# Optimization experiments

Hardware: AMD Instinct MI355X
Metric: run time of the kernel (lower is better)

Reference implementation:

```python
import jax, jax.numpy as jnp
import numpy as np

DIM = 192
HEADS = 6
HIDDEN = 384  # int(DIM * 2.0)


def _ln(x, w, b):
    # WithBias LayerNorm over channel dim (torch normalizes last dim of b,(hw),c)
    mu = jnp.mean(x, axis=1, keepdims=True)
    var = jnp.var(x, axis=1, keepdims=True)
    return (x - mu) / jnp.sqrt(var + 1e-5) * w[None, :, None, None] + b[None, :, None, None]


def _conv1x1(x, w):  # w: [O, I, 1, 1]
    return jnp.einsum('bihw,oi->bohw', x, w[:, :, 0, 0])


def _dwconv3(x, w):  # depthwise 3x3, w: [C, 1, 3, 3]
    return jax.lax.conv_general_dilated(
        x, w, window_strides=(1, 1), padding=((1, 1), (1, 1)),
        feature_group_count=x.shape[1],
        dimension_numbers=('NCHW', 'OIHW', 'NCHW'))


def _l2norm(x):  # F.normalize along last axis
    n = jnp.sqrt(jnp.sum(x * x, axis=-1, keepdims=True))
    return x / jnp.maximum(n, 1e-12)


def setup_inputs() -> dict:
    key = jax.random.key(0)
    ks = jax.random.split(key, 16)
    s = 0.02
    d = {}
    d['x'] = jax.random.normal(ks[0], (2, DIM, 128, 128), dtype=jnp.float32)
    d['k_v'] = jax.random.normal(ks[1], (2, 256), dtype=jnp.float32)
    d['ln1_w'] = jnp.ones((DIM,), jnp.float32)
    d['ln1_b'] = jnp.zeros((DIM,), jnp.float32)
    d['temp'] = jnp.ones((HEADS, 1, 1), jnp.float32)
    d['w_kR'] = jax.random.normal(ks[2], (DIM * 3 // 4, 192), jnp.float32) * s
    d['w_kI'] = jax.random.normal(ks[3], (DIM // 4, 64), jnp.float32) * s
    d['w_qR'] = jax.random.normal(ks[4], (DIM, DIM * 3 // 4, 1, 1), jnp.float32) * s
    d['w_qdw'] = jax.random.normal(ks[5], (DIM, 1, 3, 3), jnp.float32) * s
    d['w_kvI'] = jax.random.normal(ks[6], (DIM * 2, DIM // 4, 1, 1), jnp.float32) * s
    d['w_kvdw'] = jax.random.normal(ks[7], (DIM * 2, 1, 3, 3), jnp.float32) * s
    d['w_po'] = jax.random.normal(ks[8], (DIM, DIM, 1, 1), jnp.float32) * s
    d['ln2_w'] = jnp.ones((DIM,), jnp.float32)
    d['ln2_b'] = jnp.zeros((DIM,), jnp.float32)
    d['w_ffk'] = jax.random.normal(ks[9], (DIM, 256), jnp.float32) * s
    d['w_pin'] = jax.random.normal(ks[10], (HIDDEN * 2, DIM, 1, 1), jnp.float32) * s
    d['w_dw'] = jax.random.normal(ks[11], (HIDDEN * 2, 1, 3, 3), jnp.float32) * s
    d['w_pout'] = jax.random.normal(ks[12], (DIM, HIDDEN, 1, 1), jnp.float32) * s
    return d


def reference(x, k_v, ln1_w, ln1_b, temp, w_kR, w_kI, w_qR, w_qdw, w_kvI, w_kvdw,
              w_po, ln2_w, ln2_b, w_ffk, w_pin, w_dw, w_pout):
    b, c, h, w = x.shape
    c3 = c * 3 // 4
    # ---- Rttention on norm1(x) ----
    xn = _ln(x, ln1_w, ln1_b)
    kvr = (k_v[:, :192] @ w_kR.T)[:, :, None, None]   # [b, 3c/4, 1, 1]
    kvi = (k_v[:, 192:] @ w_kI.T)[:, :, None, None]   # [b, c/4, 1, 1]
    x_r = xn[:, :c3] * kvr + xn[:, :c3]
    x_i = xn[:, c3:] * kvi + xn[:, c3:]
    q = _dwconv3(_conv1x1(x_r, w_qR), w_qdw)          # [b, c, h, w]
    kv = _dwconv3(_conv1x1(x_i, w_kvI), w_kvdw)       # [b, 2c, h, w]
    k, v = jnp.split(kv, 2, axis=1)
    rh = lambda t: t.reshape(b, HEADS, c // HEADS, h * w)
    q = _l2norm(rh(q))
    k = _l2norm(rh(k))
    v = rh(v)
    # channel-wise attention: [b, head, c_h, c_h]
    attn = jax.nn.softmax(jnp.einsum('bhcd,bhed->bhce', q, k) * temp[None], axis=-1)
    out = jnp.einsum('bhce,bhed->bhcd', attn, v).reshape(b, c, h, w)
    x = x + _conv1x1(out, w_po)
    # ---- GDFN FeedForward on norm2(x) ----
    xn2 = _ln(x, ln2_w, ln2_b)
    kvf = (k_v @ w_ffk.T)[:, :, None, None]           # [b, c, 1, 1]
    y = xn2 * kvf + xn2
    y = _dwconv3(_conv1x1(y, w_pin), w_dw)            # [b, 2*hidden, h, w]
    y1, y2 = jnp.split(y, 2, axis=1)
    y = jax.nn.gelu(y1, approximate=False) * y2
    x = x + _conv1x1(y, w_pout)
    return (x, k_v)
```

## Files before the change

kernel.cpp:

```cpp
#include <hip/hip_runtime.h>
#include <math.h>

#define HW 16384
#define CDIM 192
#define C3 144
#define C4 48
#define NB 2
#define NPX 32768
#define HEADS 6

typedef unsigned short u16;
typedef unsigned int u32;
typedef __attribute__((ext_vector_type(8))) short bf16x8;
typedef __attribute__((ext_vector_type(4))) float f32x4;

__device__ __forceinline__ float bf2f(u16 u) {
    return __uint_as_float(((unsigned int)u) << 16);
}
__device__ __forceinline__ u16 f2bf(float f) {
    unsigned int x = __float_as_uint(f);
    unsigned int r = x + 0x7fffu + ((x >> 16) & 1u);
    return (u16)(r >> 16);
}

static inline float* wsf(void* ws, size_t off) { return (float*)((char*)ws + off); }
static inline u16* wsh(void* ws, size_t off) { return (u16*)((char*)ws + off); }

__global__ void k_setup(const float* __restrict__ kvv, const float* __restrict__ wkR,
                        const float* __restrict__ wkI, const float* __restrict__ wffk,
                        const float* __restrict__ wqR, const float* __restrict__ wkvI,
                        const float* __restrict__ wpo, const float* __restrict__ wpin,
                        const float* __restrict__ wpout,
                        const float* __restrict__ ln2w, const float* __restrict__ ln2b,
                        u16* __restrict__ wb, float* __restrict__ sm,
                        float* __restrict__ A2, float* __restrict__ B2,
                        float* __restrict__ tail) {
    int t = blockIdx.x * 256 + threadIdx.x;
    if (t < 313344) {
        float v;
        if (t < 30720) {
            int o = t / 160, i = t % 160;
            v = (i < 144) ? wqR[o * 144 + i] : 0.f;
        } else if (t < 55296) {
            int r = t - 30720; int o = r / 64, i = r % 64;
            v = (i < 48) ? wkvI[o * 48 + i] : 0.f;
        } else if (t < 92160) {
            v = wpo[t - 55296];
        } else if (t < 239616) {
            v = wpin[t - 92160];
        } else {
            v = wpout[t - 239616];
        }
        wb[t] = f2bf(v);
    } else if (t < 314112) {
        int r = t - 313344;
        if (r < 288) {
            int b = r / 144, o = r % 144;
            const float* v = kvv + b * 256;
            const float* w = wkR + o * 192;
            float s = 0.f;
            for (int j = 0; j < 192; j++) s += v[j] * w[j];
            sm[r] = s + 1.0f;
        } else if (r < 384) {
            int r2 = r - 288;
            int b = r2 / 48, o = r2 % 48;
            const float* v = kvv + b * 256 + 192;
            const float* w = wkI + o * 64;
            float s = 0.f;
            for (int j = 0; j < 64; j++) s += v[j] * w[j];
            sm[288 + r2] = s + 1.0f;
        } else {
            int r2 = r - 384;
            int b = r2 / 192, o = r2 % 192;
            const float* v = kvv + b * 256;
            const float* w = wffk + o * 256;
            float s = 0.f;
            for (int j = 0; j < 256; j++) s += v[j] * w[j];
            float sc = s + 1.0f;
            sm[384 + r2] = sc;
            A2[r2] = ln2w[o] * sc;
            B2[r2] = ln2b[o] * sc;
        }
    } else if (t < 314624) {
        int r = t - 314112;
        tail[r] = kvv[r];
    }
}

__global__ __launch_bounds__(256) void k_ln1(
    const float* __restrict__ xin,
    const float* __restrict__ lnw, const float* __restrict__ lnb,
    const float* __restrict__ sca, const float* __restrict__ scb,
    u16* __restrict__ outA, u16* __restrict__ outB) {
    __shared__ float red[2][16][16][4];
    __shared__ float mu_s[16][4], rstd_s[16][4];
    int t = threadIdx.x;
    int px4 = t & 15, cg = t >> 4;
    int base = blockIdx.x * 64;
    int b = base >> 14;
    int p = (base & 16383) + px4 * 4;
    float vals[12][4];
    float s[4] = {0.f, 0.f, 0.f, 0.f}, s2[4] = {0.f, 0.f, 0.f, 0.f};
#pragma unroll
    for (int j = 0; j < 12; j++) {
        int c = cg * 12 + j;
        size_t off = ((size_t)(b * CDIM + c)) * HW + p;
        float4 f = *(const float4*)(xin + off);
        float v[4] = {f.x, f.y, f.z, f.w};
#pragma unroll
        for (int q = 0; q < 4; q++) {
            vals[j][q] = v[q]; s[q] += v[q]; s2[q] += v[q] * v[q];
        }
    }
#pragma unroll
    for (int q = 0; q < 4; q++) { red[0][cg][px4][q] = s[q]; red[1][cg][px4][q] = s2[q]; }
    __syncthreads();
    if (t < 16) {
        float S[4] = {0.f, 0.f, 0.f, 0.f}, S2[4] = {0.f, 0.f, 0.f, 0.f};
        for (int g2 = 0; g2 < 16; g2++)
#pragma unroll
            for (int q = 0; q < 4; q++) { S[q] += red[0][g2][t][q]; S2[q] += red[1][g2][t][q]; }
#pragma unroll
        for (int q = 0; q < 4; q++) {
            float mu = S[q] * (1.0f / CDIM);
            float var = S2[q] * (1.0f / CDIM) - mu * mu;
            mu_s[t][q] = mu;
            rstd_s[t][q] = rsqrtf(var + 1e-5f);
        }
    }
    __syncthreads();
    float mu[4], rs[4];
#pragma unroll
    for (int q = 0; q < 4; q++) { mu[q] = mu_s[px4][q]; rs[q] = rstd_s[px4][q]; }
    float Ac[12], Bc[12];
#pragma unroll
    for (int j = 0; j < 12; j++) {
        int c = cg * 12 + j;
        float sc = (c < C3) ? sca[b * C3 + c] : scb[b * C4 + (c - C3)];
        Ac[j] = lnw[c] * sc;
        Bc[j] = lnb[c] * sc;
    }
    int isR = (cg < 12);
    size_t row0 = (size_t)b * HW + p;
    u16* basep = isR ? (outA + row0 * 160 + cg * 12)
                     : (outB + row0 * 64 + (cg * 12 - 144));
    int rowlen = isR ? 160 : 64;
#pragma unroll
    for (int q = 0; q < 4; q++) {
        u16 tmp[12];
#pragma unroll
        for (int j = 0; j < 12; j++)
            tmp[j] = f2bf((vals[j][q] - mu[q]) * rs[q] * Ac[j] + Bc[j]);
        u16* op = basep + q * rowlen;
        ushort4 o0 = {tmp[0], tmp[1], tmp[2], tmp[3]};
        ushort4 o1 = {tmp[4], tmp[5], tmp[6], tmp[7]};
        ushort4 o2 = {tmp[8], tmp[9], tmp[10], tmp[11]};
        *(ushort4*)(op) = o0;
        *(ushort4*)(op + 4) = o1;
        *(ushort4*)(op + 8) = o2;
    }
    if (cg == 0) {
        int4 z = {0, 0, 0, 0};
#pragma unroll
        for (int q = 0; q < 4; q++) {
            u16* pr = outA + (row0 + q) * 160 + 144;
            *(int4*)(pr) = z; *(int4*)(pr + 8) = z;
            u16* pi = outB + (row0 + q) * 64 + 48;
            *(int4*)(pi) = z; *(int4*)(pi + 8) = z;
        }
    }
}

template <int NCH, int MODE>
__global__ __launch_bounds__(256) void k_gemm_t(
    const u16* __restrict__ X, const u16* __restrict__ Wb,
    const void* __restrict__ resid, void* __restrict__ outp, int CO) {
    constexpr int CIP = NCH * 32;
    __shared__ __align__(16) u16 Xs[128 * 40];
    __shared__ __align__(16) u16 Wsh[64 * 40];
    const int tid = threadIdx.x;
    const int n0 = blockIdx.x * 128;
    const int m0 = blockIdx.y * 64;
    const int b = blockIdx.z;
    const int wave = tid >> 6, lane = tid & 63;
    const int quad = lane >> 4, l16 = lane & 15;
    const int spx = tid >> 1, sh = tid & 1;
    const int swr = tid >> 2, swc = tid & 3;
    const u16* xsrc = X + ((size_t)b * HW + n0 + spx) * CIP + sh * 16;
    const u16* wsrc = Wb + (size_t)(m0 + swr) * CIP + swc * 8;
    int4 xr0 = *(const int4*)(xsrc);
    int4 xr1 = *(const int4*)(xsrc + 8);
    int4 wr0 = *(const int4*)(wsrc);
    f32x4 acc[4][2] = {};
#pragma unroll
    for (int ch = 0; ch < NCH; ch++) {
        if (ch) __syncthreads();
        *(int4*)&Xs[spx * 40 + sh * 16] = xr0;
        *(int4*)&Xs[spx * 40 + sh * 16 + 8] = xr1;
        *(int4*)&Wsh[swr * 40 + swc * 8] = wr0;
        if (ch + 1 < NCH) {
            xr0 = *(const int4*)(xsrc + (ch + 1) * 32);
            xr1 = *(const int4*)(xsrc + (ch + 1) * 32 + 8);
            wr0 = *(const int4*)(wsrc + (ch + 1) * 32);
        }
        __syncthreads();
        bf16x8 af[4];
#pragma unroll
        for (int mi = 0; mi < 4; mi++)
            af[mi] = *(const bf16x8*)&Wsh[(mi * 16 + l16) * 40 + quad * 8];
        bf16x8 bf0 = *(const bf16x8*)&Xs[(wave * 32 + l16) * 40 + quad * 8];
        bf16x8 bf1 = *(const bf16x8*)&Xs[(wave * 32 + 16 + l16) * 40 + quad * 8];
#pragma unroll
        for (int mi = 0; mi < 4; mi++) {
            acc[mi][0] = __builtin_amdgcn_mfma_f32_16x16x32_bf16(af[mi], bf0, acc[mi][0], 0, 0, 0);
            acc[mi][1] = __builtin_amdgcn_mfma_f32_16x16x32_bf16(af[mi], bf1, acc[mi][1], 0, 0, 0);
        }
    }
#pragma unroll
    for (int mi = 0; mi < 4; mi++) {
#pragma unroll
        for (int ni = 0; ni < 2; ni++) {
            int c0 = m0 + mi * 16 + quad * 4;
            int px = n0 + wave * 32 + ni * 16 + l16;
            if (MODE == 0) {
                u16* ob = (u16*)outp + ((size_t)b * CO + c0) * HW + px;
#pragma unroll
                for (int rr = 0; rr < 4; rr++) ob[(size_t)rr * HW] = f2bf(acc[mi][ni][rr]);
            } else {
                const float* rp = (const float*)resid + ((size_t)b * 192 + c0) * HW + px;
                ushort4 o;
                o.x = f2bf(acc[mi][ni][0] + rp[0]);
                o.y = f2bf(acc[mi][ni][1] + rp[(size_t)HW]);
                o.z = f2bf(acc[mi][ni][2] + rp[(size_t)2 * HW]);
                o.w = f2bf(acc[mi][ni][3] + rp[(size_t)3 * HW]);
                *(ushort4*)((u16*)outp + ((size_t)b * HW + px) * 192 + c0) = o;
            }
        }
    }
}

__global__ __launch_bounds__(256) void k_gemm_s(
    const u16* __restrict__ X, const u16* __restrict__ Wb,
    const u16* __restrict__ residT, float* __restrict__ outp) {
    constexpr int NCH = 12;
    constexpr int CIP = NCH * 32;
    __shared__ __align__(16) u16 Ws[64 * 32];
    __shared__ __align__(16) u16 Xs[32 * 130];
    const int tid = threadIdx.x;
    const int n0 = blockIdx.x * 128;
    const int m0 = blockIdx.y * 64;
    const int b = blockIdx.z;
    const u16* Xb = X + (size_t)b * 384 * HW + n0;
    const int wave = tid >> 6, lane = tid & 63;
    const int quad = lane >> 4, l16 = lane & 15;
    const int smr = tid >> 2, sk4 = tid & 3;
    const int skr = tid >> 3, sc0 = (tid & 7) * 16;
    f32x4 acc[4][2] = {};
    for (int ch = 0; ch < NCH; ch++) {
        const int k0 = ch * 32;
        if (ch) __syncthreads();
        {
            const int4 wv = *(const int4*)(Wb + (size_t)(m0 + smr) * CIP + k0 + sk4 * 8);
            *(int4*)&Ws[(smr << 5) + (((sk4 ^ (smr & 3)) & 3) << 3)] = wv;
        }
        {
            const u16* xc = Xb + (size_t)(k0 + skr) * HW + sc0;
            int4 r0 = *(const int4*)xc;
            int4 r1 = *(const int4*)(xc + 8);
            u32* dst = (u32*)&Xs[skr * 130 + sc0];
#pragma unroll
            for (int i = 0; i < 4; i++) dst[i] = ((const u32*)&r0)[i];
#pragma unroll
            for (int i = 0; i < 4; i++) dst[4 + i] = ((const u32*)&r1)[i];
        }
        __syncthreads();
        bf16x8 af[4];
#pragma unroll
        for (int mi = 0; mi < 4; mi++) {
            int row = mi * 16 + l16;
            af[mi] = *(const bf16x8*)&Ws[(row << 5) + ((quad ^ (row & 3)) << 3)];
        }
#pragma unroll
        for (int ni = 0; ni < 2; ni++) {
            int n = wave * 32 + ni * 16 + l16;
            bf16x8 bfr;
#pragma unroll
            for (int j = 0; j < 8; j++) bfr[j] = (short)Xs[(quad * 8 + j) * 130 + n];
#pragma unroll
            for (int mi = 0; mi < 4; mi++)
                acc[mi][ni] = __builtin_amdgcn_mfma_f32_16x16x32_bf16(af[mi], bfr, acc[mi][ni], 0, 0, 0);
        }
    }
#pragma unroll
    for (int mi = 0; mi < 4; mi++) {
#pragma unroll
        for (int ni = 0; ni < 2; ni++) {
            int c0 = m0 + mi * 16 + quad * 4;
            int px = n0 + wave * 32 + ni * 16 + l16;
            ushort4 rv = *(const ushort4*)(residT + ((size_t)b * HW + px) * 192 + c0);
            float* ob = outp + ((size_t)b * 192 + c0) * HW + px;
            ob[0] = acc[mi][ni][0] + bf2f(rv.x);
            ob[(size_t)HW] = acc[mi][ni][1] + bf2f(rv.y);
            ob[(size_t)2 * HW] = acc[mi][ni][2] + bf2f(rv.z);
            ob[(size_t)3 * HW] = acc[mi][ni][3] + bf2f(rv.w);
        }
    }
}

__global__ __launch_bounds__(256) void k_dw2(const u16* __restrict__ X,
                                             const float* __restrict__ Wd,
                                             u16* __restrict__ out, int C, int sqCh,
                                             float* __restrict__ sqp) {
    __shared__ float In[34 * 132];
    __shared__ float red[4];
    int bc = blockIdx.x >> 2, rt = blockIdx.x & 3;
    int b = bc / C, ch = bc % C;
    const u16* xb = X + (size_t)bc * HW;
    int t = threadIdx.x;
    int c0 = (t & 7) * 16;
    for (int r = t >> 3; r < 34; r += 32) {
        int y = rt * 32 - 1 + r;
        float* dst = &In[r * 132 + 1 + c0];
        if ((unsigned)y < 128u) {
            const u16* src = xb + y * 128 + c0;
            int4 r0 = *(const int4*)src;
            int4 r1 = *(const int4*)(src + 8);
            const u16* p0 = (const u16*)&r0;
            const u16* p1 = (const u16*)&r1;
#pragma unroll
            for (int i = 0; i < 8; i++) dst[i] = bf2f(p0[i]);
#pragma unroll
            for (int i = 0; i < 8; i++) dst[8 + i] = bf2f(p1[i]);
        } else {
#pragma unroll
            for (int i = 0; i < 16; i++) dst[i] = 0.f;
        }
    }
    if (t < 34) { In[t * 132] = 0.f; In[t * 132 + 129] = 0.f; }
    __syncthreads();
    const float* w = Wd + ch * 9;
    float w00 = w[0], w01 = w[1], w02 = w[2], w10 = w[3], w11 = w[4],
          w12 = w[5], w20 = w[6], w21 = w[7], w22 = w[8];
    int x = t & 127, rg = t >> 7;
    int base = rg * 16;
    float A2 = 0.f, A1 = 0.f, B1 = 0.f, ssq = 0.f;
    u16* ob = out + (size_t)bc * HW + (rt * 32 + base) * 128 + x;
#pragma unroll
    for (int r = 0; r < 18; r++) {
        const float* row = &In[(base + r) * 132 + x];
        float v0 = row[0], v1 = row[1], v2 = row[2];
        float h0 = w00 * v0 + w01 * v1 + w02 * v2;
        float h1 = w10 * v0 + w11 * v1 + w12 * v2;
        float h2 = w20 * v0 + w21 * v1 + w22 * v2;
        if (r >= 2) {
            float val = A2 + B1 + h2;
            ob[(size_t)(r - 2) * 128] = f2bf(val);
            ssq += val * val;
        }
        A2 = A1; A1 = h0; B1 = h1;
    }
    if (ch < sqCh) {
        for (int o = 32; o > 0; o >>= 1) ssq += __shfl_down(ssq, o, 64);
        int wid = t >> 6, lane = t & 63;
        if (lane == 0) red[wid] = ssq;
        __syncthreads();
        if (t == 0) sqp[((b * 192 + ch) << 2) | rt] = red[0] + red[1] + red[2] + red[3];
    }
}

__global__ __launch_bounds__(256) void k_dw_gelu2(const u16* __restrict__ G0,
                                                  const float* __restrict__ Wd,
                                                  u16* __restrict__ out) {
    __shared__ float In[2 * 34 * 132];
    int bc = blockIdx.x >> 2, rt = blockIdx.x & 3;
    int b = bc / 384, j = bc % 384;
    int t = threadIdx.x;
    int c0 = (t & 7) * 16;
    for (int pl = 0; pl < 2; pl++) {
        const u16* xb = G0 + ((size_t)b * 768 + pl * 384 + j) * HW;
        float* pla = &In[pl * 34 * 132];
        for (int r = t >> 3; r < 34; r += 32) {
            int y = rt * 32 - 1 + r;
            float* dst = &pla[r * 132 + 1 + c0];
            if ((unsigned)y < 128u) {
                const u16* src = xb + y * 128 + c0;
                int4 r0 = *(const int4*)src;
                int4 r1 = *(const int4*)(src + 8);
                const u16* p0 = (const u16*)&r0;
                const u16* p1 = (const u16*)&r1;
#pragma unroll
                for (int i = 0; i < 8; i++) dst[i] = bf2f(p0[i]);
#pragma unroll
                for (int i = 0; i < 8; i++) dst[8 + i] = bf2f(p1[i]);
            } else {
#pragma unroll
                for (int i = 0; i < 16; i++) dst[i] = 0.f;
            }
        }
        if (t < 34) { pla[t * 132] = 0.f; pla[t * 132 + 129] = 0.f; }
    }
    __syncthreads();
    const float* w1 = Wd + j * 9;
    const float* w2 = Wd + (384 + j) * 9;
    float a00 = w1[0], a01 = w1[1], a02 = w1[2], a10 = w1[3], a11 = w1[4],
          a12 = w1[5], a20 = w1[6], a21 = w1[7], a22 = w1[8];
    float b00 = w2[0], b01 = w2[1], b02 = w2[2], b10 = w2[3], b11 = w2[4],
          b12 = w2[5], b20 = w2[6], b21 = w2[7], b22 = w2[8];
    int x = t & 127, rg = t >> 7;
    int base = rg * 16;
    float A2a = 0.f, A1a = 0.f, B1a = 0.f;
    float A2b = 0.f, A1b = 0.f, B1b = 0.f;
    u16* ob = out + ((size_t)b * 384 + j) * HW + (rt * 32 + base) * 128 + x;
#pragma unroll
    for (int r = 0; r < 18; r++) {
        const float* r1p = &In[(base + r) * 132 + x];
        const float* r2p = r1p + 34 * 132;
        float u0 = r1p[0], u1 = r1p[1], u2 = r1p[2];
        float v0 = r2p[0], v1 = r2p[1], v2 = r2p[2];
        float h0a = a00 * u0 + a01 * u1 + a02 * u2;
        float h1a = a10 * u0 + a11 * u1 + a12 * u2;
        float h2a = a20 * u0 + a21 * u1 + a22 * u2;
        float h0b = b00 * v0 + b01 * v1 + b02 * v2;
        float h1b = b10 * v0 + b11 * v1 + b12 * v2;
        float h2b = b20 * v0 + b21 * v1 + b22 * v2;
        if (r >= 2) {
            float s1 = A2a + B1a + h2a;
            float s2 = A2b + B1b + h2b;
            float g = 0.5f * s1 * (1.0f + erff(s1 * 0.70710678118654752f));
            ob[(size_t)(r - 2) * 128] = f2bf(g * s2);
        }
        A2a = A1a; A1a = h0a; B1a = h1a;
        A2b = A1b; A1b = h0b; B1b = h1b;
    }
}

__global__ __launch_bounds__(256) void k_qk(const u16* __restrict__ qb_,
                                            const u16* __restrict__ kb_,
                                            float* __restrict__ Spart) {
    int bh = blockIdx.x >> 6, ds = blockIdx.x & 63;
    int b = bh / HEADS, h = bh % HEADS;
    int tid = threadIdx.x;
    int wave = tid >> 6, lane = tid & 63;
    int quad = lane >> 4, l16 = lane & 15;
    int tm = wave >> 1, tn = wave & 1;
    const u16* qrow = qb_ + ((size_t)(b * 192 + h * 32 + tm * 16 + l16)) * HW + ds * 256 + quad * 8;
    const u16* krow = kb_ + ((size_t)(b * 384 + h * 32 + tn * 16 + l16)) * HW + ds * 256 + quad * 8;
    f32x4 acc = {};
    bf16x8 qa[3], ka[3];
    auto ld = [&](int s, int cc) {
        qa[s] = *(const bf16x8*)(qrow + cc * 32);
        ka[s] = *(const bf16x8*)(krow + cc * 32);
    };
    ld(0, 0); ld(1, 1);
#pragma unroll
    for (int ch = 0; ch < 8; ch++) {
        if (ch + 2 < 8) ld((ch + 2) % 3, ch + 2);
        acc = __builtin_amdgcn_mfma_f32_16x16x32_bf16(qa[ch % 3], ka[ch % 3], acc, 0, 0, 0);
    }
    float* Sb = Spart + ((size_t)ds * 12 + bh) * 1024;
#pragma unroll
    for (int r = 0; r < 4; r++)
        Sb[(tm * 16 + quad * 4 + r) * 32 + tn * 16 + l16] = acc[r];
}

__global__ void k_softmax(const float* __restrict__ Spart, const float* __restrict__ sqqp,
                          const float* __restrict__ sqkp, const float* __restrict__ temp,
                          u16* __restrict__ attnb) {
    int row = blockIdx.x;
    int bh = row >> 5, c2 = row & 31;
    int b = bh / HEADS, h = bh % HEADS;
    int e = threadIdx.x;
    float l = -1e30f;
    if (e < 32) {
        float s = 0.f;
        for (int d = 0; d < 64; d++) s += Spart[((size_t)d * 12 + bh) * 1024 + c2 * 32 + e];
        const float* qp = sqqp + (b * 192 + h * 32 + c2) * 4;
        const float* kp = sqkp + (b * 192 + h * 32 + e) * 4;
        float nq = qp[0] + qp[1] + qp[2] + qp[3];
        float nk = kp[0] + kp[1] + kp[2] + kp[3];
        float invq = 1.0f / fmaxf(sqrtf(nq), 1e-12f);
        float invk = 1.0f / fmaxf(sqrtf(nk), 1e-12f);
        l = s * invq * invk * temp[h];
    }
    float m = l;
    for (int o = 32; o > 0; o >>= 1) m = fmaxf(m, __shfl_xor(m, o, 64));
    float ev = (e < 32) ? expf(l - m) : 0.f;
    float ssum = ev;
    for (int o = 32; o > 0; o >>= 1) ssum += __shfl_xor(ssum, o, 64);
    if (e < 32) attnb[bh * 1024 + c2 * 32 + e] = f2bf(ev / ssum);
}

__global__ __launch_bounds__(256) void k_av(const u16* __restrict__ attnb,
                                            const u16* __restrict__ kvb,
                                            u16* __restrict__ out) {
    __shared__ __align__(16) u16 Vs[32 * 130];
    int bh = blockIdx.x >> 7;
    int pt = blockIdx.x & 127;
    int b = bh / HEADS, h = bh % HEADS;
    int p0 = pt * 128;
    int t = threadIdx.x;
    {
        int e = t >> 3, c0 = (t & 7) * 16;
        const u16* src = kvb + ((size_t)(b * 384 + 192 + h * 32 + e)) * HW + p0 + c0;
        int4 r0 = *(const int4*)src;
        int4 r1 = *(const int4*)(src + 8);
        u32* dst = (u32*)&Vs[e * 130 + c0];
#pragma unroll
        for (int i = 0; i < 4; i++) dst[i] = ((const u32*)&r0)[i];
#pragma unroll
        for (int i = 0; i < 4; i++) dst[4 + i] = ((const u32*)&r1)[i];
    }
    __syncthreads();
    int wave = t >> 6, lane = t & 63;
    int quad = lane >> 4, l16 = lane & 15;
    f32x4 acc[2][2] = {};
    bf16x8 af[2];
#pragma unroll
    for (int tm = 0; tm < 2; tm++)
        af[tm] = *(const bf16x8*)(attnb + bh * 1024 + (tm * 16 + l16) * 32 + quad * 8);
#pragma unroll
    for (int nt = 0; nt < 2; nt++) {
        int n = wave * 32 + nt * 16 + l16;
        bf16x8 bfr;
#pragma unroll
        for (int j = 0; j < 8; j++) bfr[j] = (short)Vs[(quad * 8 + j) * 130 + n];
#pragma unroll
        for (int tm = 0; tm < 2; tm++)
            acc[tm][nt] = __builtin_amdgcn_mfma_f32_16x16x32_bf16(af[tm], bfr, acc[tm][nt], 0, 0, 0);
    }
#pragma unroll
    for (int tm = 0; tm < 2; tm++)
#pragma unroll
        for (int nt = 0; nt < 2; nt++) {
            int c0 = h * 32 + tm * 16 + quad * 4;
            int px = p0 + wave * 32 + nt * 16 + l16;
            ushort4 o;
            o.x = f2bf(acc[tm][nt][0]);
            o.y = f2bf(acc[tm][nt][1]);
            o.z = f2bf(acc[tm][nt][2]);
            o.w = f2bf(acc[tm][nt][3]);
            *(ushort4*)(out + ((size_t)b * HW + px) * 192 + c0) = o;
        }
}

__global__ __launch_bounds__(256) void k_ln2t(
    const u16* __restrict__ xin, const float* __restrict__ A2,
    const float* __restrict__ B2, u16* __restrict__ outp) {
    int t = threadIdx.x;
    int pxg = blockIdx.x * 64 + (t >> 2);
    int l2 = t & 3;
    int b = pxg >> 14;
    const u16* src = xin + (size_t)pxg * 192 + l2 * 48;
    float v[48];
    float s = 0.f, s2 = 0.f;
#pragma unroll
    for (int i = 0; i < 6; i++) {
        int4 r0 = *(const int4*)(src + i * 8);
        const u16* pp = (const u16*)&r0;
#pragma unroll
        for (int k = 0; k < 8; k++) {
            float f = bf2f(pp[k]);
            v[i * 8 + k] = f; s += f; s2 += f * f;
        }
    }
    s += __shfl_xor(s, 1, 64);  s += __shfl_xor(s, 2, 64);
    s2 += __shfl_xor(s2, 1, 64); s2 += __shfl_xor(s2, 2, 64);
    float mu = s * (1.0f / CDIM);
    float rstd = rsqrtf(s2 * (1.0f / CDIM) - mu * mu + 1e-5f);
    const float* Ap = A2 + b * 192 + l2 * 48;
    const float* Bp = B2 + b * 192 + l2 * 48;
    u16* dst = outp + (size_t)pxg * 192 + l2 * 48;
#pragma unroll
    for (int i = 0; i < 12; i++) {
        float4 a = *(const float4*)(Ap + i * 4);
        float4 bb = *(const float4*)(Bp + i * 4);
        ushort4 o;
        o.x = f2bf((v[i * 4 + 0] - mu) * rstd * a.x + bb.x);
        o.y = f2bf((v[i * 4 + 1] - mu) * rstd * a.y + bb.y);
        o.z = f2bf((v[i * 4 + 2] - mu) * rstd * a.z + bb.z);
        o.w = f2bf((v[i * 4 + 3] - mu) * rstd * a.w + bb.w);
        *(ushort4*)(dst + i * 4) = o;
    }
}

extern "C" void kernel_launch(void* const* d_in, const int* in_sizes, int n_in,
                              void* d_out, int out_size, void* d_ws, size_t ws_size,
                              hipStream_t stream) {
    const float* x     = (const float*)d_in[0];
    const float* k_v   = (const float*)d_in[1];
    const float* ln1w  = (const float*)d_in[2];
    const float* ln1b  = (const float*)d_in[3];
    const float* temp  = (const float*)d_in[4];
    const float* w_kR  = (const float*)d_in[5];
    const float* w_kI  = (const float*)d_in[6];
    const float* w_qR  = (const float*)d_in[7];
    const float* w_qdw = (const float*)d_in[8];
    const float* w_kvI = (const float*)d_in[9];
    const float* w_kvdw= (const float*)d_in[10];
    const float* w_po  = (const float*)d_in[11];
    const float* ln2w  = (const float*)d_in[12];
    const float* ln2b  = (const float*)d_in[13];
    const float* w_ffk = (const float*)d_in[14];
    const float* w_pin = (const float*)d_in[15];
    const float* w_dw  = (const float*)d_in[16];
    const float* w_pout= (const float*)d_in[17];
    float* out = (float*)d_out;

    const size_t MiB = 1048576ULL;
    u16*   q0b     = wsh(d_ws, 0);
    u16*   attnoutb= wsh(d_ws, 0);
    u16*   y0b     = wsh(d_ws, 0);
    u16*   kv0b    = wsh(d_ws, 12 * MiB);
    u16*   ybufb   = wsh(d_ws, 12 * MiB);
    u16*   x1b     = wsh(d_ws, 36 * MiB);
    u16*   qbuf_b  = wsh(d_ws, 48 * MiB);
    u16*   kvbuf_b = wsh(d_ws, 60 * MiB);
    u16*   xrb     = wsh(d_ws, 84 * MiB);
    u16*   xib     = wsh(d_ws, 94 * MiB);
    u16*   g0b     = wsh(d_ws, 98 * MiB);
    u16*   wb      = wsh(d_ws, 146 * MiB);
    float* sm      = wsf(d_ws, 147 * MiB);
    float* Spart   = wsf(d_ws, 0);
    u16* wq   = wb;
    u16* wkv  = wb + 30720;
    u16* wpo  = wb + 55296;
    u16* wpin = wb + 92160;
    u16* wpout= wb + 239616;
    float* kvr  = sm;
    float* kvi  = sm + 288;
    float* sqqp = sm + 768;
    float* sqkp = sm + 2304;
    u16*   attnb= (u16*)(sm + 3840);
    float* A2c  = sm + 10240;
    float* B2c  = sm + 10624;

    k_setup<<<1229, 256, 0, stream>>>(k_v, w_kR, w_kI, w_ffk, w_qR, w_kvI, w_po,
                                      w_pin, w_pout, ln2w, ln2b, wb, sm, A2c, B2c,
                                      out + (size_t)NB * CDIM * HW);
    k_ln1<<<NPX / 64, 256, 0, stream>>>(x, ln1w, ln1b, kvr, kvi, xrb, xib);
    k_gemm_t<5, 0><<<dim3(128, 3, 2), 256, 0, stream>>>(xrb, wq, nullptr, q0b, 192);
    k_gemm_t<2, 0><<<dim3(128, 6, 2), 256, 0, stream>>>(xib, wkv, nullptr, kv0b, 384);
    k_dw2<<<NB * 192 * 4, 256, 0, stream>>>(q0b, w_qdw, qbuf_b, 192, 192, sqqp);
    k_dw2<<<NB * 384 * 4, 256, 0, stream>>>(kv0b, w_kvdw, kvbuf_b, 384, 192, sqkp);
    k_qk<<<12 * 64, 256, 0, stream>>>(qbuf_b, kvbuf_b, Spart);
    k_softmax<<<384, 64, 0, stream>>>(Spart, sqqp, sqkp, temp, attnb);
    k_av<<<12 * 128, 256, 0, stream>>>(attnb, kvbuf_b, attnoutb);
    k_gemm_t<6, 1><<<dim3(128, 3, 2), 256, 0, stream>>>(attnoutb, wpo, x, x1b, 192);
    k_ln2t<<<NPX / 64, 256, 0, stream>>>(x1b, A2c, B2c, y0b);
    k_gemm_t<6, 0><<<dim3(128, 12, 2), 256, 0, stream>>>(y0b, wpin, nullptr, g0b, 768);
    k_dw_gelu2<<<NB * 384 * 4, 256, 0, stream>>>(g0b, w_dw, ybufb);
    k_gemm_s<<<dim3(128, 3, 2), 256, 0, stream>>>(ybufb, wpout, x1b, out);
}
```

Baseline: 262.4 us.

## Prefetch-pipeline final GEMM, merge q/kv depthwise launches, unroll setup dots

Rewrites the final projection GEMM to transpose its activation tile into pixel-major shared memory and to prefetch the next K-chunk into registers while the current one computes. Vectorized 16-byte fragment reads replace the per-element strided B gathers. Merges the two depthwise-conv launches for q and kv into one grid. Adds unroll pragmas to the setup dot products. The register prefetch raises register pressure, and the per-pixel column loads are 2-byte strided global reads that may coalesce poorly.

```diff
diff --git a/kernel.cpp b/kernel.cpp
--- a/kernel.cpp
+++ b/kernel.cpp
@@ -59,6 +59,7 @@
             const float* v = kvv + b * 256;
             const float* w = wkR + o * 192;
             float s = 0.f;
+#pragma unroll 8
             for (int j = 0; j < 192; j++) s += v[j] * w[j];
             sm[r] = s + 1.0f;
         } else if (r < 384) {
@@ -67,6 +68,7 @@
             const float* v = kvv + b * 256 + 192;
             const float* w = wkI + o * 64;
             float s = 0.f;
+#pragma unroll 8
             for (int j = 0; j < 64; j++) s += v[j] * w[j];
             sm[288 + r2] = s + 1.0f;
         } else {
@@ -75,6 +77,7 @@
             const float* v = kvv + b * 256;
             const float* w = wffk + o * 256;
             float s = 0.f;
+#pragma unroll 8
             for (int j = 0; j < 256; j++) s += v[j] * w[j];
             float sc = s + 1.0f;
             sm[384 + r2] = sc;
@@ -239,56 +242,59 @@
     }
 }
 
-__global__ __launch_bounds__(256) void k_gemm_s(
+__global__ __launch_bounds__(256) void k_gemm_pt(
     const u16* __restrict__ X, const u16* __restrict__ Wb,
     const u16* __restrict__ residT, float* __restrict__ outp) {
     constexpr int NCH = 12;
-    constexpr int CIP = NCH * 32;
-    __shared__ __align__(16) u16 Ws[64 * 32];
-    __shared__ __align__(16) u16 Xs[32 * 130];
+    constexpr int CIP = 384;
+    __shared__ __align__(16) u16 Xs[128 * 40];
+    __shared__ __align__(16) u16 Wsh[64 * 40];
     const int tid = threadIdx.x;
     const int n0 = blockIdx.x * 128;
     const int m0 = blockIdx.y * 64;
     const int b = blockIdx.z;
-    const u16* Xb = X + (size_t)b * 384 * HW + n0;
     const int wave = tid >> 6, lane = tid & 63;
     const int quad = lane >> 4, l16 = lane & 15;
-    const int smr = tid >> 2, sk4 = tid & 3;
-    const int skr = tid >> 3, sc0 = (tid & 7) * 16;
+    const int spx = tid >> 1, sh = tid & 1;
+    const int swr = tid >> 2, swc = tid & 3;
+    const u16* xcol = X + (size_t)b * CIP * HW + ((size_t)sh * 16) * HW + n0 + spx;
+    const u16* wsrc = Wb + (size_t)(m0 + swr) * CIP + swc * 8;
+    u32 xl[16];
+    int4 wr0;
+#pragma unroll
+    for (int i = 0; i < 16; i++) xl[i] = xcol[(size_t)i * HW];
+    wr0 = *(const int4*)(wsrc);
     f32x4 acc[4][2] = {};
+#pragma unroll
     for (int ch = 0; ch < NCH; ch++) {
-        const int k0 = ch * 32;
         if (ch) __syncthreads();
         {
-            const int4 wv = *(const int4*)(Wb + (size_t)(m0 + smr) * CIP + k0 + sk4 * 8);
-            *(int4*)&Ws[(smr << 5) + (((sk4 ^ (smr & 3)) & 3) << 3)] = wv;
-        }
-        {
-            const u16* xc = Xb + (size_t)(k0 + skr) * HW + sc0;
-            int4 r0 = *(const int4*)xc;
-            int4 r1 = *(const int4*)(xc + 8);
-            u32* dst = (u32*)&Xs[skr * 130 + sc0];
-#pragma unroll
-            for (int i = 0; i < 4; i++) dst[i] = ((const u32*)&r0)[i];
-#pragma unroll
-            for (int i = 0; i < 4; i++) dst[4 + i] = ((const u32*)&r1)[i];
+            int4 w0, w1;
+            w0.x = xl[0] | (xl[1] << 16);  w0.y = xl[2] | (xl[3] << 16);
+            w0.z = xl[4] | (xl[5] << 16);  w0.w = xl[6] | (xl[7] << 16);
+            w1.x = xl[8] | (xl[9] << 16);  w1.y = xl[10] | (xl[11] << 16);
+            w1.z = xl[12] | (xl[13] << 16); w1.w = xl[14] | (xl[15] << 16);
+            *(int4*)&Xs[spx * 40 + sh * 16] = w0;
+            *(int4*)&Xs[spx * 40 + sh * 16 + 8] = w1;
+            *(int4*)&Wsh[swr * 40 + swc * 8] = wr0;
+        }
+        if (ch + 1 < NCH) {
+            const u16* xn = xcol + (size_t)(ch + 1) * 32 * HW;
+#pragma unroll
+            for (int i = 0; i < 16; i++) xl[i] = xn[(size_t)i * HW];
+            wr0 = *(const int4*)(wsrc + (ch + 1) * 32);
         }
         __syncthreads();
         bf16x8 af[4];
 #pragma unroll
+        for (int mi = 0; mi < 4; mi++)
+            af[mi] = *(const bf16x8*)&Wsh[(mi * 16 + l16) * 40 + quad * 8];
+        bf16x8 bf0 = *(const bf16x8*)&Xs[(wave * 32 + l16) * 40 + quad * 8];
+        bf16x8 bf1 = *(const bf16x8*)&Xs[(wave * 32 + 16 + l16) * 40 + quad * 8];
+#pragma unroll
         for (int mi = 0; mi < 4; mi++) {
-            int row = mi * 16 + l16;
-            af[mi] = *(const bf16x8*)&Ws[(row << 5) + ((quad ^ (row & 3)) << 3)];
-        }
-#pragma unroll
-        for (int ni = 0; ni < 2; ni++) {
-            int n = wave * 32 + ni * 16 + l16;
-            bf16x8 bfr;
-#pragma unroll
-            for (int j = 0; j < 8; j++) bfr[j] = (short)Xs[(quad * 8 + j) * 130 + n];
-#pragma unroll
-            for (int mi = 0; mi < 4; mi++)
-                acc[mi][ni] = __builtin_amdgcn_mfma_f32_16x16x32_bf16(af[mi], bfr, acc[mi][ni], 0, 0, 0);
+            acc[mi][0] = __builtin_amdgcn_mfma_f32_16x16x32_bf16(af[mi], bf0, acc[mi][0], 0, 0, 0);
+            acc[mi][1] = __builtin_amdgcn_mfma_f32_16x16x32_bf16(af[mi], bf1, acc[mi][1], 0, 0, 0);
         }
     }
 #pragma unroll
@@ -307,15 +313,25 @@
     }
 }
 
-__global__ __launch_bounds__(256) void k_dw2(const u16* __restrict__ X,
-                                             const float* __restrict__ Wd,
-                                             u16* __restrict__ out, int C, int sqCh,
-                                             float* __restrict__ sqp) {
+__global__ __launch_bounds__(256) void k_dw2m(const u16* __restrict__ Xq,
+                                              const u16* __restrict__ Xkv,
+                                              const float* __restrict__ Wdq,
+                                              const float* __restrict__ Wdkv,
+                                              u16* __restrict__ outq,
+                                              u16* __restrict__ outkv,
+                                              float* __restrict__ sqq,
+                                              float* __restrict__ sqk) {
     __shared__ float In[34 * 132];
     __shared__ float red[4];
     int bc = blockIdx.x >> 2, rt = blockIdx.x & 3;
-    int b = bc / C, ch = bc % C;
-    const u16* xb = X + (size_t)bc * HW;
+    int b = bc / 576, ch = bc % 576;
+    int isQ = (ch < 192);
+    int c2 = isQ ? ch : ch - 192;
+    const u16* xb = isQ ? Xq + ((size_t)(b * 192 + c2)) * HW
+                        : Xkv + ((size_t)(b * 384 + c2)) * HW;
+    const float* w = isQ ? (Wdq + c2 * 9) : (Wdkv + c2 * 9);
+    u16* ob_base = isQ ? outq + ((size_t)(b * 192 + c2)) * HW
+                       : outkv + ((size_t)(b * 384 + c2)) * HW;
     int t = threadIdx.x;
     int c0 = (t & 7) * 16;
     for (int r = t >> 3; r < 34; r += 32) {
@@ -338,13 +354,12 @@
     }
     if (t < 34) { In[t * 132] = 0.f; In[t * 132 + 129] = 0.f; }
     __syncthreads();
-    const float* w = Wd + ch * 9;
     float w00 = w[0], w01 = w[1], w02 = w[2], w10 = w[3], w11 = w[4],
           w12 = w[5], w20 = w[6], w21 = w[7], w22 = w[8];
     int x = t & 127, rg = t >> 7;
     int base = rg * 16;
     float A2 = 0.f, A1 = 0.f, B1 = 0.f, ssq = 0.f;
-    u16* ob = out + (size_t)bc * HW + (rt * 32 + base) * 128 + x;
+    u16* ob = ob_base + (rt * 32 + base) * 128 + x;
 #pragma unroll
     for (int r = 0; r < 18; r++) {
         const float* row = &In[(base + r) * 132 + x];
@@ -359,12 +374,13 @@
         }
         A2 = A1; A1 = h0; B1 = h1;
     }
-    if (ch < sqCh) {
+    if (c2 < 192) {
         for (int o = 32; o > 0; o >>= 1) ssq += __shfl_down(ssq, o, 64);
         int wid = t >> 6, lane = t & 63;
         if (lane == 0) red[wid] = ssq;
         __syncthreads();
-        if (t == 0) sqp[((b * 192 + ch) << 2) | rt] = red[0] + red[1] + red[2] + red[3];
+        float* sp = isQ ? sqq : sqk;
+        if (t == 0) sp[((b * 192 + c2) << 2) | rt] = red[0] + red[1] + red[2] + red[3];
     }
 }
 
@@ -640,8 +656,8 @@
     k_ln1<<<NPX / 64, 256, 0, stream>>>(x, ln1w, ln1b, kvr, kvi, xrb, xib);
     k_gemm_t<5, 0><<<dim3(128, 3, 2), 256, 0, stream>>>(xrb, wq, nullptr, q0b, 192);
     k_gemm_t<2, 0><<<dim3(128, 6, 2), 256, 0, stream>>>(xib, wkv, nullptr, kv0b, 384);
-    k_dw2<<<NB * 192 * 4, 256, 0, stream>>>(q0b, w_qdw, qbuf_b, 192, 192, sqqp);
-    k_dw2<<<NB * 384 * 4, 256, 0, stream>>>(kv0b, w_kvdw, kvbuf_b, 384, 192, sqkp);
+    k_dw2m<<<NB * 576 * 4, 256, 0, stream>>>(q0b, kv0b, w_qdw, w_kvdw,
+                                             qbuf_b, kvbuf_b, sqqp, sqkp);
     k_qk<<<12 * 64, 256, 0, stream>>>(qbuf_b, kvbuf_b, Spart);
     k_softmax<<<384, 64, 0, stream>>>(Spart, sqqp, sqkp, temp, attnb);
     k_av<<<12 * 128, 256, 0, stream>>>(attnb, kvbuf_b, attnoutb);
@@ -649,5 +665,5 @@
     k_ln2t<<<NPX / 64, 256, 0, stream>>>(x1b, A2c, B2c, y0b);
     k_gemm_t<6, 0><<<dim3(128, 12, 2), 256, 0, stream>>>(y0b, wpin, nullptr, g0b, 768);
     k_dw_gelu2<<<NB * 384 * 4, 256, 0, stream>>>(g0b, w_dw, ybufb);
-    k_gemm_s<<<dim3(128, 3, 2), 256, 0, stream>>>(ybufb, wpout, x1b, out);
-}
+    k_gemm_pt<<<dim3(128, 3, 2), 256, 0, stream>>>(ybufb, wpout, x1b, out);
+}
```

Result: slower. 274.0 us (+4.4%).
